# Kernel tuning notes

Measured on AMD Instinct MI355X. Metric: run time of the kernel, lower is better.

Reference implementation:

```python
import jax, jax.numpy as jnp
import numpy as np

ALPHA = 0.99
EPS = 1e-14


def setup_inputs() -> dict:
    key = jax.random.key(0)
    B, C, T, F = 16, 1, 2000, 481
    x = jax.random.normal(key, (B, C, T, F, 2), dtype=jnp.float32)
    # unit_norm_init: linearly decaying initial norm state over freq bins
    init_state = jnp.linspace(0.001, 0.0001, F, dtype=jnp.float32).reshape(1, 1, F, 1)
    return {"x": x, "init_state": init_state}


def reference(x, init_state):
    # x: [B, C, T, F, 2] (real/imag), init_state: [1, 1, F, 1]
    B, C, T, F, _ = x.shape
    # complex magnitude per (b,c,t,f), clamped for stability: [B, C, T, F, 1]
    x_abs = jnp.sqrt(jnp.maximum(jnp.sum(x * x, axis=-1, keepdims=True), EPS))
    # scan over time: state = (1-alpha)*|x_t| + alpha*state
    xs = jnp.moveaxis(x_abs, 2, 0)  # [T, B, C, F, 1]
    s0 = jnp.broadcast_to(init_state, (B, C, F, 1)).astype(x.dtype)

    def step(s, xt):
        s = xt * (1.0 - ALPHA) + s * ALPHA
        return s, s

    _, states = jax.lax.scan(step, s0, xs)  # [T, B, C, F, 1]
    states = jnp.moveaxis(states, 0, 2)  # [B, C, T, F, 1]
    return x / jnp.sqrt(states)
```

## Files before the change

### kernel.cpp

```cpp
#include <hip/hip_runtime.h>


#define ALPHA_F 0.99f
#define OMA_F   0.01f
#define EPS_F   1e-14f

constexpr int Bn = 16;
constexpr int Tn = 2000;
constexpr int Fn = 481;
constexpr int NC = 50;
constexpr int L  = Tn / NC;
constexpr int UN = 10;
constexpr int W  = 24;
#define ALPHA_L 0.668971758f

__global__ __launch_bounds__(256) void eun_pass1(
    const float* __restrict__ x, float* __restrict__ part) {
  const int f = blockIdx.x * blockDim.x + threadIdx.x;
  if (f >= Fn) return;
  const int b = blockIdx.y;
  const int c = blockIdx.z;

  const size_t stride = (size_t)Fn * 2;
  const float* xp = x + ((size_t)b * Tn + (size_t)c * L) * stride + (size_t)f * 2;

  float s = 0.f;
  for (int t0 = 0; t0 < L; t0 += UN) {
    float2 v[UN];
#pragma unroll
    for (int j = 0; j < UN; ++j)
      v[j] = *(const float2*)(xp + (size_t)j * stride);
#pragma unroll
    for (int j = 0; j < UN; ++j) {
      float m = sqrtf(fmaxf(fmaf(v[j].x, v[j].x, v[j].y * v[j].y), EPS_F));
      s = fmaf(ALPHA_F, s, OMA_F * m);
    }
    xp += (size_t)UN * stride;
  }
  part[((size_t)b * NC + c) * Fn + f] = s;
}

__global__ __launch_bounds__(256) void eun_pass2(
    const float* __restrict__ x, const float* __restrict__ part,
    const float* __restrict__ init_state, float* __restrict__ out) {
  const int f = blockIdx.x * blockDim.x + threadIdx.x;
  if (f >= Fn) return;
  const int b = blockIdx.y;
  const int c = blockIdx.z;

  const float* pb = part + (size_t)b * NC * Fn + f;
  const int n = (c < W) ? c : W;
  float pv[W];
#pragma unroll
  for (int k = 0; k < W; ++k)
    if (k < n) pv[k] = pb[(size_t)(c - 1 - k) * Fn];
  float s = 0.f, w = 1.f;
#pragma unroll
  for (int k = 0; k < W; ++k)
    if (k < n) { s = fmaf(w, pv[k], s); w *= ALPHA_L; }
  if (c <= W) s = fmaf(w, init_state[f], s);

  const size_t stride = (size_t)Fn * 2;
  const size_t off = ((size_t)b * Tn + (size_t)c * L) * stride + (size_t)f * 2;
  const float* xp = x + off;
  float*       op = out + off;

  for (int t0 = 0; t0 < L; t0 += UN) {
    float2 v[UN];
#pragma unroll
    for (int j = 0; j < UN; ++j)
      v[j] = *(const float2*)(xp + (size_t)j * stride);
#pragma unroll
    for (int j = 0; j < UN; ++j) {
      float m = sqrtf(fmaxf(fmaf(v[j].x, v[j].x, v[j].y * v[j].y), EPS_F));
      s = fmaf(ALPHA_F, s, OMA_F * m);
      float inv = rsqrtf(s);
      *(float2*)(op + (size_t)j * stride) = make_float2(v[j].x * inv, v[j].y * inv);
    }
    xp += (size_t)UN * stride;
    op += (size_t)UN * stride;
  }
}

extern "C" void kernel_launch(void* const* d_in, const int* in_sizes, int n_in,
                              void* d_out, int out_size, void* d_ws, size_t ws_size,
                              hipStream_t stream) {
  const float* x    = (const float*)d_in[0];
  const float* init = (const float*)d_in[1];
  float* out        = (float*)d_out;
  float* part       = (float*)d_ws;

  dim3 grid((Fn + 255) / 256, Bn, NC);
  eun_pass1<<<grid, dim3(256), 0, stream>>>(x, part);
  eun_pass2<<<grid, dim3(256), 0, stream>>>(x, part, init, out);
}
```

Baseline: 255.5 us.

## Stage time tiles through LDS with float4 coalesced loads and nontemporal stores

Each block now covers one (batch, chunk) pair across all 481 frequency bins. It copies 8-timestep tiles into shared memory with fully contiguous float4 loads, runs the per-frequency scan out of LDS with two bins per thread, and in pass 2 writes the normalized tile back to LDS before streaming it out with nontemporal float4 stores. The goal is to replace the old strided float2 accesses and partly idle 256-thread blocks (481 bins split over two blocks) with wide coalesced transfers. In exchange it adds two or three barriers per tile and cuts the grid to 800 blocks, which may lower occupancy and latency hiding.

```diff
diff --git a/kernel.cpp b/kernel.cpp
--- a/kernel.cpp
+++ b/kernel.cpp
@@ -5,80 +5,138 @@
 #define OMA_F   0.01f
 #define EPS_F   1e-14f
 
+typedef float f32x4 __attribute__((ext_vector_type(4)));
+
 constexpr int Bn = 16;
 constexpr int Tn = 2000;
 constexpr int Fn = 481;
 constexpr int NC = 50;
 constexpr int L  = Tn / NC;
-constexpr int UN = 10;
+constexpr int ST = 8;
+constexpr int NS = L / ST;
+constexpr int F4S = ST * Fn / 2;
+constexpr int TAIL = F4S - 7 * 256;
 constexpr int W  = 24;
 #define ALPHA_L 0.668971758f
 
 __global__ __launch_bounds__(256) void eun_pass1(
     const float* __restrict__ x, float* __restrict__ part) {
-  const int f = blockIdx.x * blockDim.x + threadIdx.x;
-  if (f >= Fn) return;
-  const int b = blockIdx.y;
-  const int c = blockIdx.z;
+  __shared__ float4 lds[F4S];
+  const int tid = threadIdx.x;
+  const int c = blockIdx.x, b = blockIdx.y;
 
-  const size_t stride = (size_t)Fn * 2;
-  const float* xp = x + ((size_t)b * Tn + (size_t)c * L) * stride + (size_t)f * 2;
+  const float4* xb = (const float4*)x + (size_t)(b * 500 + c * 10) * 962;
 
-  float s = 0.f;
-  for (int t0 = 0; t0 < L; t0 += UN) {
-    float2 v[UN];
+  const int f1 = tid;
+  const int f2 = tid + 256;
+  float s1 = 0.f, s2 = 0.f;
+
+  for (int st = 0; st < NS; ++st) {
+    const float4* sb = xb + st * F4S;
+    float4 v[8];
 #pragma unroll
-    for (int j = 0; j < UN; ++j)
-      v[j] = *(const float2*)(xp + (size_t)j * stride);
+    for (int j = 0; j < 7; ++j) v[j] = sb[tid + 256 * j];
+    if (tid < TAIL) v[7] = sb[tid + 256 * 7];
 #pragma unroll
-    for (int j = 0; j < UN; ++j) {
-      float m = sqrtf(fmaxf(fmaf(v[j].x, v[j].x, v[j].y * v[j].y), EPS_F));
-      s = fmaf(ALPHA_F, s, OMA_F * m);
+    for (int j = 0; j < 7; ++j) lds[tid + 256 * j] = v[j];
+    if (tid < TAIL) lds[tid + 256 * 7] = v[7];
+    __syncthreads();
+
+    const float2* l2 = (const float2*)lds;
+#pragma unroll
+    for (int t = 0; t < ST; ++t) {
+      float2 a = l2[t * Fn + f1];
+      float m = sqrtf(fmaxf(fmaf(a.x, a.x, a.y * a.y), EPS_F));
+      s1 = fmaf(ALPHA_F, s1, OMA_F * m);
+      if (f2 < Fn) {
+        float2 q = l2[t * Fn + f2];
+        float m2 = sqrtf(fmaxf(fmaf(q.x, q.x, q.y * q.y), EPS_F));
+        s2 = fmaf(ALPHA_F, s2, OMA_F * m2);
+      }
     }
-    xp += (size_t)UN * stride;
+    __syncthreads();
   }
-  part[((size_t)b * NC + c) * Fn + f] = s;
+  float* pp = part + ((size_t)b * NC + c) * Fn;
+  pp[f1] = s1;
+  if (f2 < Fn) pp[f2] = s2;
 }
 
 __global__ __launch_bounds__(256) void eun_pass2(
     const float* __restrict__ x, const float* __restrict__ part,
     const float* __restrict__ init_state, float* __restrict__ out) {
-  const int f = blockIdx.x * blockDim.x + threadIdx.x;
-  if (f >= Fn) return;
-  const int b = blockIdx.y;
-  const int c = blockIdx.z;
+  __shared__ float4 lds[F4S];
+  const int tid = threadIdx.x;
+  const int c = blockIdx.x, b = blockIdx.y;
 
-  const float* pb = part + (size_t)b * NC * Fn + f;
+  const size_t cb = (size_t)(b * 500 + c * 10) * 962;
+  const float4* xb = (const float4*)x + cb;
+  f32x4*        ob = (f32x4*)out + cb;
+
+  const int f1 = tid, f2 = tid + 256;
+
+  const float* pb = part + (size_t)b * NC * Fn;
   const int n = (c < W) ? c : W;
-  float pv[W];
+  float pv1[W], pv2[W];
 #pragma unroll
   for (int k = 0; k < W; ++k)
-    if (k < n) pv[k] = pb[(size_t)(c - 1 - k) * Fn];
-  float s = 0.f, w = 1.f;
+    if (k < n) {
+      pv1[k] = pb[(size_t)(c - 1 - k) * Fn + f1];
+      if (f2 < Fn) pv2[k] = pb[(size_t)(c - 1 - k) * Fn + f2];
+    }
+  float s1 = 0.f, s2 = 0.f, w = 1.f;
 #pragma unroll
   for (int k = 0; k < W; ++k)
-    if (k < n) { s = fmaf(w, pv[k], s); w *= ALPHA_L; }
-  if (c <= W) s = fmaf(w, init_state[f], s);
+    if (k < n) {
+      s1 = fmaf(w, pv1[k], s1);
+      if (f2 < Fn) s2 = fmaf(w, pv2[k], s2);
+      w *= ALPHA_L;
+    }
+  if (c <= W) {
+    s1 = fmaf(w, init_state[f1], s1);
+    if (f2 < Fn) s2 = fmaf(w, init_state[f2], s2);
+  }
 
-  const size_t stride = (size_t)Fn * 2;
-  const size_t off = ((size_t)b * Tn + (size_t)c * L) * stride + (size_t)f * 2;
-  const float* xp = x + off;
-  float*       op = out + off;
+  for (int st = 0; st < NS; ++st) {
+    const float4* sb = xb + st * F4S;
+    float4 v[8];
+#pragma unroll
+    for (int j = 0; j < 7; ++j) v[j] = sb[tid + 256 * j];
+    if (tid < TAIL) v[7] = sb[tid + 256 * 7];
+#pragma unroll
+    for (int j = 0; j < 7; ++j) lds[tid + 256 * j] = v[j];
+    if (tid < TAIL) lds[tid + 256 * 7] = v[7];
+    __syncthreads();
 
-  for (int t0 = 0; t0 < L; t0 += UN) {
-    float2 v[UN];
+    float2* l2 = (float2*)lds;
 #pragma unroll
-    for (int j = 0; j < UN; ++j)
-      v[j] = *(const float2*)(xp + (size_t)j * stride);
+    for (int t = 0; t < ST; ++t) {
+      float2 a = l2[t * Fn + f1];
+      float m = sqrtf(fmaxf(fmaf(a.x, a.x, a.y * a.y), EPS_F));
+      s1 = fmaf(ALPHA_F, s1, OMA_F * m);
+      float inv1 = rsqrtf(s1);
+      l2[t * Fn + f1] = make_float2(a.x * inv1, a.y * inv1);
+      if (f2 < Fn) {
+        float2 q = l2[t * Fn + f2];
+        float m2 = sqrtf(fmaxf(fmaf(q.x, q.x, q.y * q.y), EPS_F));
+        s2 = fmaf(ALPHA_F, s2, OMA_F * m2);
+        float inv2 = rsqrtf(s2);
+        l2[t * Fn + f2] = make_float2(q.x * inv2, q.y * inv2);
+      }
+    }
+    __syncthreads();
+
+    f32x4* obs = ob + st * F4S;
+    const f32x4* ls = (const f32x4*)lds;
 #pragma unroll
-    for (int j = 0; j < UN; ++j) {
-      float m = sqrtf(fmaxf(fmaf(v[j].x, v[j].x, v[j].y * v[j].y), EPS_F));
-      s = fmaf(ALPHA_F, s, OMA_F * m);
-      float inv = rsqrtf(s);
-      *(float2*)(op + (size_t)j * stride) = make_float2(v[j].x * inv, v[j].y * inv);
+    for (int j = 0; j < 7; ++j) {
+      f32x4 o = ls[tid + 256 * j];
+      __builtin_nontemporal_store(o, obs + tid + 256 * j);
     }
-    xp += (size_t)UN * stride;
-    op += (size_t)UN * stride;
+    if (tid < TAIL) {
+      f32x4 o = ls[tid + 256 * 7];
+      __builtin_nontemporal_store(o, obs + tid + 256 * 7);
+    }
+    __syncthreads();
   }
 }
 
@@ -90,7 +148,7 @@
   float* out        = (float*)d_out;
   float* part       = (float*)d_ws;
 
-  dim3 grid((Fn + 255) / 256, Bn, NC);
+  dim3 grid(NC, Bn);
   eun_pass1<<<grid, dim3(256), 0, stream>>>(x, part);
   eun_pass2<<<grid, dim3(256), 0, stream>>>(x, part, init, out);
 }
```

Measured after the change: 291.2 us. 1.14x slower.

## Fuse chunked scan passes into one cooperative kernel with grid-wide sync

Applied to the files above, without the earlier changes.

Merges the two chunked-scan passes into a single cooperative kernel. Each block computes its chunk's partial state, waits at a grid-wide barrier, then combines earlier chunk partials and writes the normalized output. This is meant to remove the second launch and its gap, and to reread x soon enough that it may still sit in cache. Output stores become nontemporal so they do not evict x. If occupancy is too low for a cooperative launch, it falls back to a three-kernel path: a finer 100-chunk first pass, a sequential prefix over chunk partials, then the normalize pass. The risks are the grid-sync cost and the occupancy requirement of the cooperative launch.

```diff
diff --git a/kernel.cpp b/kernel.cpp
--- a/kernel.cpp
+++ b/kernel.cpp
@@ -1,4 +1,7 @@
 #include <hip/hip_runtime.h>
+#include <hip/hip_cooperative_groups.h>
+
+namespace cg = cooperative_groups;
 
 
 #define ALPHA_F 0.99f
@@ -14,57 +17,52 @@
 constexpr int W  = 24;
 #define ALPHA_L 0.668971758f
 
-__global__ __launch_bounds__(256) void eun_pass1(
-    const float* __restrict__ x, float* __restrict__ part) {
-  const int f = blockIdx.x * blockDim.x + threadIdx.x;
-  if (f >= Fn) return;
+__global__ __launch_bounds__(256, 7) void eun_coop(
+    const float* __restrict__ x, const float* __restrict__ init_state,
+    float* __restrict__ out, float* __restrict__ part) {
+  const int f = blockIdx.x * 256 + threadIdx.x;
   const int b = blockIdx.y;
   const int c = blockIdx.z;
+  const bool act = (f < Fn);
 
   const size_t stride = (size_t)Fn * 2;
-  const float* xp = x + ((size_t)b * Tn + (size_t)c * L) * stride + (size_t)f * 2;
+  const size_t off = ((size_t)b * Tn + (size_t)c * L) * stride + (size_t)f * 2;
 
-  float s = 0.f;
-  for (int t0 = 0; t0 < L; t0 += UN) {
-    float2 v[UN];
+  if (act) {
+    const float* xp = x + off;
+    float p = 0.f;
+    for (int t0 = 0; t0 < L; t0 += UN) {
+      float2 v[UN];
 #pragma unroll
-    for (int j = 0; j < UN; ++j)
-      v[j] = *(const float2*)(xp + (size_t)j * stride);
+      for (int j = 0; j < UN; ++j)
+        v[j] = *(const float2*)(xp + (size_t)j * stride);
 #pragma unroll
-    for (int j = 0; j < UN; ++j) {
-      float m = sqrtf(fmaxf(fmaf(v[j].x, v[j].x, v[j].y * v[j].y), EPS_F));
-      s = fmaf(ALPHA_F, s, OMA_F * m);
+      for (int j = 0; j < UN; ++j) {
+        float m = sqrtf(fmaxf(fmaf(v[j].x, v[j].x, v[j].y * v[j].y), EPS_F));
+        p = fmaf(ALPHA_F, p, OMA_F * m);
+      }
+      xp += (size_t)UN * stride;
     }
-    xp += (size_t)UN * stride;
+    part[((size_t)b * NC + c) * Fn + f] = p;
   }
-  part[((size_t)b * NC + c) * Fn + f] = s;
-}
 
-__global__ __launch_bounds__(256) void eun_pass2(
-    const float* __restrict__ x, const float* __restrict__ part,
-    const float* __restrict__ init_state, float* __restrict__ out) {
-  const int f = blockIdx.x * blockDim.x + threadIdx.x;
-  if (f >= Fn) return;
-  const int b = blockIdx.y;
-  const int c = blockIdx.z;
+  cg::this_grid().sync();
+
+  if (!act) return;
 
   const float* pb = part + (size_t)b * NC * Fn + f;
   const int n = (c < W) ? c : W;
-  float pv[W];
-#pragma unroll
-  for (int k = 0; k < W; ++k)
-    if (k < n) pv[k] = pb[(size_t)(c - 1 - k) * Fn];
   float s = 0.f, w = 1.f;
 #pragma unroll
   for (int k = 0; k < W; ++k)
-    if (k < n) { s = fmaf(w, pv[k], s); w *= ALPHA_L; }
+    if (k < n) {
+      s = fmaf(w, pb[(size_t)(c - 1 - k) * Fn], s);
+      w *= ALPHA_L;
+    }
   if (c <= W) s = fmaf(w, init_state[f], s);
 
-  const size_t stride = (size_t)Fn * 2;
-  const size_t off = ((size_t)b * Tn + (size_t)c * L) * stride + (size_t)f * 2;
   const float* xp = x + off;
   float*       op = out + off;
-
   for (int t0 = 0; t0 < L; t0 += UN) {
     float2 v[UN];
 #pragma unroll
@@ -75,10 +73,82 @@
       float m = sqrtf(fmaxf(fmaf(v[j].x, v[j].x, v[j].y * v[j].y), EPS_F));
       s = fmaf(ALPHA_F, s, OMA_F * m);
       float inv = rsqrtf(s);
-      *(float2*)(op + (size_t)j * stride) = make_float2(v[j].x * inv, v[j].y * inv);
+      union { float2 f2; unsigned long long u; } cvt;
+      cvt.f2 = make_float2(v[j].x * inv, v[j].y * inv);
+      __builtin_nontemporal_store(cvt.u,
+          (unsigned long long*)(op + (size_t)j * stride));
     }
     xp += (size_t)UN * stride;
     op += (size_t)UN * stride;
+  }
+}
+
+constexpr int NCf = 100;
+constexpr int Lf  = Tn / NCf;
+constexpr int MT  = 25;
+#define ALPHA_LF 0.817906938f
+
+__global__ __launch_bounds__(256) void eun_pass1(
+    const float* __restrict__ x, float* __restrict__ part) {
+  const int f = blockIdx.x * blockDim.x + threadIdx.x;
+  if (f >= Fn) return;
+  const int b = blockIdx.y, c = blockIdx.z;
+  const size_t stride = (size_t)Fn * 2;
+  const float* xp = x + ((size_t)b * Tn + (size_t)c * Lf) * stride + (size_t)f * 2;
+  float2 v[Lf];
+#pragma unroll
+  for (int j = 0; j < Lf; ++j) v[j] = *(const float2*)(xp + (size_t)j * stride);
+  float s = 0.f;
+#pragma unroll
+  for (int j = 0; j < Lf; ++j) {
+    float m = sqrtf(fmaxf(fmaf(v[j].x, v[j].x, v[j].y * v[j].y), EPS_F));
+    s = fmaf(ALPHA_F, s, OMA_F * m);
+  }
+  part[((size_t)b * NCf + c) * Fn + f] = s;
+}
+
+__global__ __launch_bounds__(256) void eun_mid(
+    const float* __restrict__ init_state, float* __restrict__ part) {
+  const int f = blockIdx.x * blockDim.x + threadIdx.x;
+  if (f >= Fn) return;
+  const int b = blockIdx.y;
+  float* pp = part + (size_t)b * NCf * Fn + f;
+  float s = init_state[f];
+  for (int c0 = 0; c0 < NCf; c0 += MT) {
+    float p[MT];
+#pragma unroll
+    for (int k = 0; k < MT; ++k) p[k] = pp[(size_t)(c0 + k) * Fn];
+#pragma unroll
+    for (int k = 0; k < MT; ++k) {
+      pp[(size_t)(c0 + k) * Fn] = s;
+      s = fmaf(s, ALPHA_LF, p[k]);
+    }
+  }
+}
+
+__global__ __launch_bounds__(256) void eun_pass2(
+    const float* __restrict__ x, const float* __restrict__ start,
+    float* __restrict__ out) {
+  const int f = blockIdx.x * blockDim.x + threadIdx.x;
+  if (f >= Fn) return;
+  const int b = blockIdx.y, c = blockIdx.z;
+  float s = start[((size_t)b * NCf + c) * Fn + f];
+  const size_t stride = (size_t)Fn * 2;
+  const size_t off = ((size_t)b * Tn + (size_t)c * Lf) * stride + (size_t)f * 2;
+  const float* xp = x + off;
+  float*       op = out + off;
+  float2 v[Lf];
+#pragma unroll
+  for (int j = 0; j < Lf; ++j) v[j] = *(const float2*)(xp + (size_t)j * stride);
+#pragma unroll
+  for (int j = 0; j < Lf; ++j) {
+    float m = sqrtf(fmaxf(fmaf(v[j].x, v[j].x, v[j].y * v[j].y), EPS_F));
+    s = fmaf(ALPHA_F, s, OMA_F * m);
+    float inv = rsqrtf(s);
+    union { float2 f2; unsigned long long u; } cvt;
+    cvt.f2 = make_float2(v[j].x * inv, v[j].y * inv);
+    __builtin_nontemporal_store(cvt.u,
+        (unsigned long long*)(op + (size_t)j * stride));
   }
 }
 
@@ -90,7 +160,19 @@
   float* out        = (float*)d_out;
   float* part       = (float*)d_ws;
 
-  dim3 grid((Fn + 255) / 256, Bn, NC);
-  eun_pass1<<<grid, dim3(256), 0, stream>>>(x, part);
-  eun_pass2<<<grid, dim3(256), 0, stream>>>(x, part, init, out);
+  int maxB = 0;
+  (void)hipOccupancyMaxActiveBlocksPerMultiprocessor(&maxB, (const void*)eun_coop,
+                                                     256, 0);
+  const int needed = 2 * Bn * NC;
+  if (maxB * 256 >= needed) {
+    void* args[] = {(void*)&x, (void*)&init, (void*)&out, (void*)&part};
+    (void)hipLaunchCooperativeKernel((const void*)eun_coop,
+                                     dim3(2, Bn, NC), dim3(256),
+                                     args, 0, stream);
+  } else {
+    dim3 grid3((Fn + 255) / 256, Bn, NCf);
+    eun_pass1<<<grid3, dim3(256), 0, stream>>>(x, part);
+    eun_mid<<<dim3((Fn + 255) / 256, Bn), dim3(256), 0, stream>>>(init, part);
+    eun_pass2<<<grid3, dim3(256), 0, stream>>>(x, part, out);
+  }
 }
```

Result: faster. 238.4 us (-6.7%).
